# Kernel optimization log

Measured on AMD Instinct MI355X. Metric: run time of the kernel, lower is better.

Reference implementation:

```python
import jax, jax.numpy as jnp
import numpy as np
import math

N = 100000        # nodes
E = 3200000       # edges (avg degree 32)
DIN = 128         # in_features
DOUT = 64         # out_features
LAMDA = 0.5       # GCNII lambda
ALPHA = 0.1       # GCNII alpha
L = 1             # layer index


def setup_inputs() -> dict:
    key = jax.random.key(0)
    ks = jax.random.split(key, 6)
    x = jax.random.normal(ks[0], (N, DIN), dtype=jnp.float32)
    adj_rows = jnp.sort(jax.random.randint(ks[1], (E,), 0, N, dtype=jnp.int32))
    adj_cols = jax.random.randint(ks[2], (E,), 0, N, dtype=jnp.int32)
    adj_vals = jax.random.uniform(ks[3], (E,), dtype=jnp.float32)
    h0 = jax.random.normal(ks[4], (N, DOUT), dtype=jnp.float32)
    weight = jax.random.normal(ks[5], (DIN, DOUT), dtype=jnp.float32) * 0.02  # xavier-ish gain 0.02
    bias = jnp.zeros((1, DOUT), dtype=jnp.float32)
    return {"x": x, "adj_rows": adj_rows, "adj_cols": adj_cols,
            "adj_vals": adj_vals, "h0": h0, "weight": weight, "bias": bias}


def reference(x, adj_rows, adj_cols, adj_vals, h0, weight, bias):
    theta = math.log(LAMDA / L + 1)
    # dense projection: [N, DIN] @ [DIN, DOUT]
    xw = x @ weight
    # SpMM: hi[r] = sum_{e: rows[e]==r} vals[e] * xw[cols[e]]
    hi = jax.ops.segment_sum(adj_vals[:, None] * xw[adj_cols], adj_rows, num_segments=N)
    # non-variant GCNII combine
    support = (1.0 - ALPHA) * hi + ALPHA * h0
    r = support
    out = theta * support + (1.0 - theta) * r
    return out + bias
```

## Files before the change

### kernel.cpp

```cpp
#include <hip/hip_runtime.h>

#define N_NODES 100000
#define N_EDGES 3200000
#define DIN     128
#define DOUT    64
#define GEMM_BLOCKS 1563
#define RP_BLOCKS   12500

typedef unsigned short bf16_t;
typedef float f32x4  __attribute__((ext_vector_type(4)));
typedef short bf16x8 __attribute__((ext_vector_type(8)));

__device__ __forceinline__ bf16_t f32_to_bf16(float f) {
    union { float f; unsigned int u; } un; un.f = f;
    unsigned int u = un.u + 0x7fffu + ((un.u >> 16) & 1u);
    return (bf16_t)(u >> 16);
}
__device__ __forceinline__ unsigned int pack2(float lo, float hi) {
    return (unsigned int)f32_to_bf16(lo) | ((unsigned int)f32_to_bf16(hi) << 16);
}
__device__ __forceinline__ float2 bf16x2_to_f32x2(unsigned int p) {
    union { unsigned int u; float f; } lo, hi;
    lo.u = p << 16;
    hi.u = p & 0xffff0000u;
    return make_float2(lo.f, hi.f);
}

#define UNPACK_FMA(ACC, G, VV)                                    \
    do {                                                          \
        const float2 _f0 = bf16x2_to_f32x2((G).x);                \
        const float2 _f1 = bf16x2_to_f32x2((G).y);                \
        const float2 _f2 = bf16x2_to_f32x2((G).z);                \
        const float2 _f3 = bf16x2_to_f32x2((G).w);                \
        ACC[0] += (VV) * _f0.x; ACC[1] += (VV) * _f0.y;           \
        ACC[2] += (VV) * _f1.x; ACC[3] += (VV) * _f1.y;           \
        ACC[4] += (VV) * _f2.x; ACC[5] += (VV) * _f2.y;           \
        ACC[6] += (VV) * _f3.x; ACC[7] += (VV) * _f3.y;           \
    } while (0)

#define MGROUP(ACC, EBASE, END)                                             \
    do {                                                                    \
        const int   _ei = (EBASE) + grp;                                    \
        const bool  _ok = _ei < (END);                                      \
        const int   _ec = _ok ? _ei : 0;                                    \
        const int   _cc = cols[_ec];                                        \
        const float _vv = _ok ? vals[_ec] : 0.f;                            \
        const uint4 _g  = *(const uint4*)&xwb[(size_t)_cc * DOUT + 8 * fq]; \
        UNPACK_FMA(ACC, _g, _vv);                                           \
    } while (0)

__global__ __launch_bounds__(256) void gemm_rowptr(const float* __restrict__ x,
                                                   const float* __restrict__ w,
                                                   const int*   __restrict__ rows,
                                                   bf16_t* __restrict__ xwb,
                                                   int* __restrict__ row_ptr) {
    __shared__ unsigned short Xs[64][DIN];
    __shared__ unsigned short Wt[DOUT][DIN];

    const int bid = blockIdx.x;
    const int tid = threadIdx.x;

    if (bid >= GEMM_BLOCKS) {
        const int e = (bid - GEMM_BLOCKS) * 256 + tid;
        if (e < N_EDGES) {
            const int cur  = rows[e];
            const int prev = (e == 0) ? -1 : rows[e - 1];
            for (int r = prev + 1; r <= cur; ++r) row_ptr[r] = e;
            if (e == N_EDGES - 1)
                for (int r = cur + 1; r <= N_NODES; ++r) row_ptr[r] = N_EDGES;
        }
        return;
    }

    const int block_row = bid * 64;

    {
        const float4* w4 = (const float4*)w;
#pragma unroll
        for (int i = 0; i < 8; ++i) {
            const int f4 = i * 256 + tid;
            const float4 v = w4[f4];
            const int base = f4 * 4;
            const int k = base >> 6;
            const int n = base & 63;
            Wt[n + 0][(((k >> 3) ^ ((n + 0) & 7)) << 3) | (k & 7)] = f32_to_bf16(v.x);
            Wt[n + 1][(((k >> 3) ^ ((n + 1) & 7)) << 3) | (k & 7)] = f32_to_bf16(v.y);
            Wt[n + 2][(((k >> 3) ^ ((n + 2) & 7)) << 3) | (k & 7)] = f32_to_bf16(v.z);
            Wt[n + 3][(((k >> 3) ^ ((n + 3) & 7)) << 3) | (k & 7)] = f32_to_bf16(v.w);
        }
    }
    {
        const int r = tid >> 2;
        const int q = tid & 3;
        const int gr = block_row + r;
        const float4* xp = (const float4*)&x[(size_t)gr * DIN + q * 32];
        const bool ok = gr < N_NODES;
#pragma unroll
        for (int ci = 0; ci < 4; ++ci) {
            float4 a = make_float4(0.f, 0.f, 0.f, 0.f), b = a;
            if (ok) { a = xp[2 * ci]; b = xp[2 * ci + 1]; }
            uint4 pk;
            pk.x = pack2(a.x, a.y);
            pk.y = pack2(a.z, a.w);
            pk.z = pack2(b.x, b.y);
            pk.w = pack2(b.z, b.w);
            const int c = q * 4 + ci;
            *(uint4*)&Xs[r][(c ^ (r & 7)) << 3] = pk;
        }
    }
    __syncthreads();

    const int wv_ = tid >> 6;
    const int l   = tid & 63;
    const int lr  = l & 15;
    const int hi  = l >> 4;
    const int arow = wv_ * 16 + lr;

    f32x4 acc0 = {0.f, 0.f, 0.f, 0.f};
    f32x4 acc1 = acc0, acc2 = acc0, acc3 = acc0;
#pragma unroll
    for (int s = 0; s < 4; ++s) {
        const int kc = s * 4 + hi;
        const bf16x8 a  = *(const bf16x8*)&Xs[arow][(kc ^ (arow & 7)) << 3];
        const int bc = (kc ^ (lr & 7)) << 3;
        const bf16x8 b0 = *(const bf16x8*)&Wt[lr     ][bc];
        const bf16x8 b1 = *(const bf16x8*)&Wt[16 + lr][bc];
        const bf16x8 b2 = *(const bf16x8*)&Wt[32 + lr][bc];
        const bf16x8 b3 = *(const bf16x8*)&Wt[48 + lr][bc];
        acc0 = __builtin_amdgcn_mfma_f32_16x16x32_bf16(a, b0, acc0, 0, 0, 0);
        acc1 = __builtin_amdgcn_mfma_f32_16x16x32_bf16(a, b1, acc1, 0, 0, 0);
        acc2 = __builtin_amdgcn_mfma_f32_16x16x32_bf16(a, b2, acc2, 0, 0, 0);
        acc3 = __builtin_amdgcn_mfma_f32_16x16x32_bf16(a, b3, acc3, 0, 0, 0);
    }

#pragma unroll
    for (int reg = 0; reg < 4; ++reg) {
        const int grow = block_row + wv_ * 16 + hi * 4 + reg;
        if (grow < N_NODES) {
            bf16_t* o = &xwb[(size_t)grow * DOUT + lr];
            o[0]  = f32_to_bf16(acc0[reg]);
            o[16] = f32_to_bf16(acc1[reg]);
            o[32] = f32_to_bf16(acc2[reg]);
            o[48] = f32_to_bf16(acc3[reg]);
        }
    }
}

__global__ __launch_bounds__(256) void spmm_pair(const bf16_t* __restrict__ xwb,
                                                 const int*    __restrict__ row_ptr,
                                                 const int*    __restrict__ cols,
                                                 const float*  __restrict__ vals,
                                                 const float*  __restrict__ h0,
                                                 const float*  __restrict__ bias,
                                                 float* __restrict__ out) {
    const int wid  = (blockIdx.x * blockDim.x + threadIdx.x) >> 6;
    const int lane = threadIdx.x & 63;
    const int r0 = wid << 1;
    if (r0 >= N_NODES) return;

    const int grp = lane >> 3;
    const int fq  = lane & 7;

    const int s0 = __builtin_amdgcn_readfirstlane(row_ptr[r0]);
    const int m0 = __builtin_amdgcn_readfirstlane(row_ptr[r0 + 1]);
    const int e1 = __builtin_amdgcn_readfirstlane(row_ptr[r0 + 2]);

    const int rsel = r0 + (grp == 1 ? 1 : 0);
    const f32x4 ha = __builtin_nontemporal_load((const f32x4*)&h0[(size_t)rsel * DOUT + 8 * fq]);
    const f32x4 hb = __builtin_nontemporal_load((const f32x4*)&h0[(size_t)rsel * DOUT + 8 * fq + 4]);
    const f32x4 ba = *(const f32x4*)&bias[8 * fq];
    const f32x4 bb = *(const f32x4*)&bias[8 * fq + 4];

    float accA[8] = {};
    float accB[8] = {};

    MGROUP(accA, s0,      m0);  MGROUP(accB, m0,      e1);
    MGROUP(accA, s0 + 8,  m0);  MGROUP(accB, m0 + 8,  e1);
    MGROUP(accA, s0 + 16, m0);  MGROUP(accB, m0 + 16, e1);
    MGROUP(accA, s0 + 24, m0);  MGROUP(accB, m0 + 24, e1);
    MGROUP(accA, s0 + 32, m0);  MGROUP(accB, m0 + 32, e1);
    MGROUP(accA, s0 + 40, m0);  MGROUP(accB, m0 + 40, e1);

    for (int e = s0 + 48; e < m0; e += 8) MGROUP(accA, e, m0);
    for (int e = m0 + 48; e < e1; e += 8) MGROUP(accB, e, e1);

    float a0, a1, a2, a3, a4, a5, a6, a7;
    float b0, b1, b2, b3, b4, b5, b6, b7;
#define RED(ACC, J, S)                                   \
    do {                                                 \
        float _t = ACC[J];                               \
        _t += __shfl_xor(_t, 8, 64);                     \
        _t += __shfl_xor(_t, 16, 64);                    \
        _t += __shfl_xor(_t, 32, 64);                    \
        S = _t;                                          \
    } while (0)
    RED(accA, 0, a0); RED(accA, 1, a1); RED(accA, 2, a2); RED(accA, 3, a3);
    RED(accA, 4, a4); RED(accA, 5, a5); RED(accA, 6, a6); RED(accA, 7, a7);
    RED(accB, 0, b0); RED(accB, 1, b1); RED(accB, 2, b2); RED(accB, 3, b3);
    RED(accB, 4, b4); RED(accB, 5, b5); RED(accB, 6, b6); RED(accB, 7, b7);
#undef RED

    if (grp < 2) {
        const bool g1 = (grp == 1);
        const float t0 = g1 ? b0 : a0;
        const float t1 = g1 ? b1 : a1;
        const float t2 = g1 ? b2 : a2;
        const float t3 = g1 ? b3 : a3;
        const float t4 = g1 ? b4 : a4;
        const float t5 = g1 ? b5 : a5;
        const float t6 = g1 ? b6 : a6;
        const float t7 = g1 ? b7 : a7;
        f32x4 ra, rb;
        ra.x = 0.9f * t0 + 0.1f * ha.x + ba.x;
        ra.y = 0.9f * t1 + 0.1f * ha.y + ba.y;
        ra.z = 0.9f * t2 + 0.1f * ha.z + ba.z;
        ra.w = 0.9f * t3 + 0.1f * ha.w + ba.w;
        rb.x = 0.9f * t4 + 0.1f * hb.x + bb.x;
        rb.y = 0.9f * t5 + 0.1f * hb.y + bb.y;
        rb.z = 0.9f * t6 + 0.1f * hb.z + bb.z;
        rb.w = 0.9f * t7 + 0.1f * hb.w + bb.w;
        __builtin_nontemporal_store(ra, (f32x4*)&out[(size_t)rsel * DOUT + 8 * fq]);
        __builtin_nontemporal_store(rb, (f32x4*)&out[(size_t)rsel * DOUT + 8 * fq + 4]);
    }
}

extern "C" void kernel_launch(void* const* d_in, const int* in_sizes, int n_in,
                              void* d_out, int out_size, void* d_ws, size_t ws_size,
                              hipStream_t stream) {
    const float* x    = (const float*)d_in[0];
    const int*   rows = (const int*)  d_in[1];
    const int*   cols = (const int*)  d_in[2];
    const float* vals = (const float*)d_in[3];
    const float* h0   = (const float*)d_in[4];
    const float* w    = (const float*)d_in[5];
    const float* bias = (const float*)d_in[6];
    float* out = (float*)d_out;

    bf16_t* xwb = (bf16_t*)d_ws;
    const size_t xw_bytes = (size_t)N_NODES * DOUT * sizeof(bf16_t);
    int* row_ptr = (int*)((char*)d_ws + xw_bytes);

    gemm_rowptr<<<GEMM_BLOCKS + RP_BLOCKS, 256, 0, stream>>>(x, w, rows, xwb, row_ptr);
    spmm_pair<<<(N_NODES / 2 + 3) / 4, 256, 0, stream>>>(
        xwb, row_ptr, cols, vals, h0, bias, out);
}
```

Baseline: 103.7 us.

## Process 13 rows per wave serially with prefetch of next row metadata

Replaces the two-rows-per-wave SpMM kernel with a kernel where each wave walks 13 consecutive rows. It prefetches the next row's row_ptr entry and h0 slice while the current row is processed, and uses an unmasked 32-edge main loop with a masked tail. The aim is to cut per-wave launch and setup overhead and the masked-edge waste, and to overlap metadata loads with gathers. The cost is fewer waves (about 7700), so less parallelism for hiding gather latency, and rows are handled one after another within a wave.

```diff
diff --git a/kernel.cpp b/kernel.cpp
--- a/kernel.cpp
+++ b/kernel.cpp
@@ -6,6 +6,7 @@
 #define DOUT    64
 #define GEMM_BLOCKS 1563
 #define RP_BLOCKS   12500
+#define RPW 13
 
 typedef unsigned short bf16_t;
 typedef float f32x4  __attribute__((ext_vector_type(4)));
@@ -38,11 +39,11 @@
         ACC[6] += (VV) * _f3.x; ACC[7] += (VV) * _f3.y;           \
     } while (0)
 
-#define MGROUP(ACC, EBASE, END)                                             \
+#define MASKED_GROUP(ACC, EBASE)                                            \
     do {                                                                    \
         const int   _ei = (EBASE) + grp;                                    \
-        const bool  _ok = _ei < (END);                                      \
-        const int   _ec = _ok ? _ei : 0;                                    \
+        const bool  _ok = _ei < end;                                        \
+        const int   _ec = _ok ? _ei : start;                                \
         const int   _cc = cols[_ec];                                        \
         const float _vv = _ok ? vals[_ec] : 0.f;                            \
         const uint4 _g  = *(const uint4*)&xwb[(size_t)_cc * DOUT + 8 * fq]; \
@@ -146,81 +147,105 @@
     }
 }
 
-__global__ __launch_bounds__(256) void spmm_pair(const bf16_t* __restrict__ xwb,
-                                                 const int*    __restrict__ row_ptr,
-                                                 const int*    __restrict__ cols,
-                                                 const float*  __restrict__ vals,
-                                                 const float*  __restrict__ h0,
-                                                 const float*  __restrict__ bias,
-                                                 float* __restrict__ out) {
+__global__ __launch_bounds__(256) void spmm_persist(const bf16_t* __restrict__ xwb,
+                                                    const int*    __restrict__ row_ptr,
+                                                    const int*    __restrict__ cols,
+                                                    const float*  __restrict__ vals,
+                                                    const float*  __restrict__ h0,
+                                                    const float*  __restrict__ bias,
+                                                    float* __restrict__ out) {
     const int wid  = (blockIdx.x * blockDim.x + threadIdx.x) >> 6;
     const int lane = threadIdx.x & 63;
-    const int r0 = wid << 1;
-    if (r0 >= N_NODES) return;
+
+    int r = wid * RPW;
+    if (r >= N_NODES) return;
+    const int rend = (r + RPW < N_NODES) ? (r + RPW) : N_NODES;
 
     const int grp = lane >> 3;
     const int fq  = lane & 7;
 
-    const int s0 = __builtin_amdgcn_readfirstlane(row_ptr[r0]);
-    const int m0 = __builtin_amdgcn_readfirstlane(row_ptr[r0 + 1]);
-    const int e1 = __builtin_amdgcn_readfirstlane(row_ptr[r0 + 2]);
-
-    const int rsel = r0 + (grp == 1 ? 1 : 0);
-    const f32x4 ha = __builtin_nontemporal_load((const f32x4*)&h0[(size_t)rsel * DOUT + 8 * fq]);
-    const f32x4 hb = __builtin_nontemporal_load((const f32x4*)&h0[(size_t)rsel * DOUT + 8 * fq + 4]);
     const f32x4 ba = *(const f32x4*)&bias[8 * fq];
     const f32x4 bb = *(const f32x4*)&bias[8 * fq + 4];
 
-    float accA[8] = {};
-    float accB[8] = {};
-
-    MGROUP(accA, s0,      m0);  MGROUP(accB, m0,      e1);
-    MGROUP(accA, s0 + 8,  m0);  MGROUP(accB, m0 + 8,  e1);
-    MGROUP(accA, s0 + 16, m0);  MGROUP(accB, m0 + 16, e1);
-    MGROUP(accA, s0 + 24, m0);  MGROUP(accB, m0 + 24, e1);
-    MGROUP(accA, s0 + 32, m0);  MGROUP(accB, m0 + 32, e1);
-    MGROUP(accA, s0 + 40, m0);  MGROUP(accB, m0 + 40, e1);
-
-    for (int e = s0 + 48; e < m0; e += 8) MGROUP(accA, e, m0);
-    for (int e = m0 + 48; e < e1; e += 8) MGROUP(accB, e, e1);
-
-    float a0, a1, a2, a3, a4, a5, a6, a7;
-    float b0, b1, b2, b3, b4, b5, b6, b7;
-#define RED(ACC, J, S)                                   \
-    do {                                                 \
-        float _t = ACC[J];                               \
-        _t += __shfl_xor(_t, 8, 64);                     \
-        _t += __shfl_xor(_t, 16, 64);                    \
-        _t += __shfl_xor(_t, 32, 64);                    \
-        S = _t;                                          \
-    } while (0)
-    RED(accA, 0, a0); RED(accA, 1, a1); RED(accA, 2, a2); RED(accA, 3, a3);
-    RED(accA, 4, a4); RED(accA, 5, a5); RED(accA, 6, a6); RED(accA, 7, a7);
-    RED(accB, 0, b0); RED(accB, 1, b1); RED(accB, 2, b2); RED(accB, 3, b3);
-    RED(accB, 4, b4); RED(accB, 5, b5); RED(accB, 6, b6); RED(accB, 7, b7);
+    int sA = row_ptr[r];
+    int eA = row_ptr[r + 1];
+    f32x4 haA = __builtin_nontemporal_load((const f32x4*)&h0[(size_t)r * DOUT + 8 * fq]);
+    f32x4 hbA = __builtin_nontemporal_load((const f32x4*)&h0[(size_t)r * DOUT + 8 * fq + 4]);
+
+    for (;;) {
+        const int rn = r + 1;
+        const bool more = rn < rend;
+        int eN = 0;
+        f32x4 haN = {0.f, 0.f, 0.f, 0.f}, hbN = haN;
+        if (more) {
+            eN  = row_ptr[rn + 1];
+            haN = __builtin_nontemporal_load((const f32x4*)&h0[(size_t)rn * DOUT + 8 * fq]);
+            hbN = __builtin_nontemporal_load((const f32x4*)&h0[(size_t)rn * DOUT + 8 * fq + 4]);
+        }
+
+        const int start = __builtin_amdgcn_readfirstlane(sA);
+        const int end   = __builtin_amdgcn_readfirstlane(eA);
+
+        float accA[8] = {};
+        float accB[8] = {};
+        if (start < end) {
+            int e = start;
+            for (; e + 32 <= end; e += 32) {
+                const int   c0 = cols[e      + grp];
+                const int   c1 = cols[e + 8  + grp];
+                const int   c2 = cols[e + 16 + grp];
+                const int   c3 = cols[e + 24 + grp];
+                const float v0 = vals[e      + grp];
+                const float v1 = vals[e + 8  + grp];
+                const float v2 = vals[e + 16 + grp];
+                const float v3 = vals[e + 24 + grp];
+                const uint4 g0 = *(const uint4*)&xwb[(size_t)c0 * DOUT + 8 * fq];
+                const uint4 g1 = *(const uint4*)&xwb[(size_t)c1 * DOUT + 8 * fq];
+                const uint4 g2 = *(const uint4*)&xwb[(size_t)c2 * DOUT + 8 * fq];
+                const uint4 g3 = *(const uint4*)&xwb[(size_t)c3 * DOUT + 8 * fq];
+                UNPACK_FMA(accA, g0, v0);
+                UNPACK_FMA(accB, g1, v1);
+                UNPACK_FMA(accA, g2, v2);
+                UNPACK_FMA(accB, g3, v3);
+            }
+            for (; e < end; e += 16) {
+                MASKED_GROUP(accA, e);
+                if (e + 8 < end) MASKED_GROUP(accB, e + 8);
+            }
+        }
+
+        float s0, s1, s2, s3, s4, s5, s6, s7;
+#define RED(SJ, J)                                       \
+        do {                                             \
+            float _t = accA[J] + accB[J];                \
+            _t += __shfl_xor(_t, 8, 64);                 \
+            _t += __shfl_xor(_t, 16, 64);                \
+            _t += __shfl_xor(_t, 32, 64);                \
+            SJ = _t;                                     \
+        } while (0)
+        RED(s0, 0); RED(s1, 1); RED(s2, 2); RED(s3, 3);
+        RED(s4, 4); RED(s5, 5); RED(s6, 6); RED(s7, 7);
 #undef RED
 
-    if (grp < 2) {
-        const bool g1 = (grp == 1);
-        const float t0 = g1 ? b0 : a0;
-        const float t1 = g1 ? b1 : a1;
-        const float t2 = g1 ? b2 : a2;
-        const float t3 = g1 ? b3 : a3;
-        const float t4 = g1 ? b4 : a4;
-        const float t5 = g1 ? b5 : a5;
-        const float t6 = g1 ? b6 : a6;
-        const float t7 = g1 ? b7 : a7;
-        f32x4 ra, rb;
-        ra.x = 0.9f * t0 + 0.1f * ha.x + ba.x;
-        ra.y = 0.9f * t1 + 0.1f * ha.y + ba.y;
-        ra.z = 0.9f * t2 + 0.1f * ha.z + ba.z;
-        ra.w = 0.9f * t3 + 0.1f * ha.w + ba.w;
-        rb.x = 0.9f * t4 + 0.1f * hb.x + bb.x;
-        rb.y = 0.9f * t5 + 0.1f * hb.y + bb.y;
-        rb.z = 0.9f * t6 + 0.1f * hb.z + bb.z;
-        rb.w = 0.9f * t7 + 0.1f * hb.w + bb.w;
-        __builtin_nontemporal_store(ra, (f32x4*)&out[(size_t)rsel * DOUT + 8 * fq]);
-        __builtin_nontemporal_store(rb, (f32x4*)&out[(size_t)rsel * DOUT + 8 * fq + 4]);
+        if (grp == 0) {
+            f32x4 ra, rb;
+            ra.x = 0.9f * s0 + 0.1f * haA.x + ba.x;
+            ra.y = 0.9f * s1 + 0.1f * haA.y + ba.y;
+            ra.z = 0.9f * s2 + 0.1f * haA.z + ba.z;
+            ra.w = 0.9f * s3 + 0.1f * haA.w + ba.w;
+            rb.x = 0.9f * s4 + 0.1f * hbA.x + bb.x;
+            rb.y = 0.9f * s5 + 0.1f * hbA.y + bb.y;
+            rb.z = 0.9f * s6 + 0.1f * hbA.z + bb.z;
+            rb.w = 0.9f * s7 + 0.1f * hbA.w + bb.w;
+            __builtin_nontemporal_store(ra, (f32x4*)&out[(size_t)r * DOUT + 8 * fq]);
+            __builtin_nontemporal_store(rb, (f32x4*)&out[(size_t)r * DOUT + 8 * fq + 4]);
+        }
+
+        if (!more) break;
+        sA = eA;
+        eA = eN;
+        haA = haN; hbA = hbN;
+        r = rn;
     }
 }
 
@@ -241,6 +266,9 @@
     int* row_ptr = (int*)((char*)d_ws + xw_bytes);
 
     gemm_rowptr<<<GEMM_BLOCKS + RP_BLOCKS, 256, 0, stream>>>(x, w, rows, xwb, row_ptr);
-    spmm_pair<<<(N_NODES / 2 + 3) / 4, 256, 0, stream>>>(
+
+    const int waves  = (N_NODES + RPW - 1) / RPW;
+    const int blocks = (waves + 3) / 4;
+    spmm_persist<<<blocks, 256, 0, stream>>>(
         xwb, row_ptr, cols, vals, h0, bias, out);
 }
```

New measurement: 115.5 us. 11.4% more time.
